# Kernel optimization log

Measured on AMD Instinct MI355X. Metric: run time of the kernel, lower is better.

The kernel has to match this reference:

```python
import jax, jax.numpy as jnp
import numpy as np

N_NODES = 100000
N_EDGES = 3200000
G_EDGES = 1600000
D_FEAT = 256
K_CLUSTERS = 16
COLLAPSE_REG = 0.1


def setup_inputs() -> dict:
    key = jax.random.key(0)
    ks = jax.random.split(key, 12)
    inp = {
        'features': jax.random.normal(ks[0], (N_NODES, D_FEAT), dtype=jnp.float32),
        'W': jax.random.normal(ks[1], (D_FEAT, K_CLUSTERS), dtype=jnp.float32) / np.sqrt(D_FEAT),
        'b': jnp.zeros((K_CLUSTERS,), dtype=jnp.float32),
        'adj_src': jax.random.randint(ks[2], (N_EDGES,), 0, N_NODES, dtype=jnp.int32),
        'adj_dst': jax.random.randint(ks[3], (N_EDGES,), 0, N_NODES, dtype=jnp.int32),
        'adj_val': jax.random.uniform(ks[4], (N_EDGES,), dtype=jnp.float32),
        'g1_src': jax.random.randint(ks[5], (G_EDGES,), 0, N_NODES, dtype=jnp.int32),
        'g1_dst': jax.random.randint(ks[6], (G_EDGES,), 0, N_NODES, dtype=jnp.int32),
        'g1_val': jax.random.uniform(ks[7], (G_EDGES,), dtype=jnp.float32),
        'g2_src': jax.random.randint(ks[8], (G_EDGES,), 0, N_NODES, dtype=jnp.int32),
        'g2_dst': jax.random.randint(ks[9], (G_EDGES,), 0, N_NODES, dtype=jnp.int32),
        'g2_val': jax.random.uniform(ks[10], (G_EDGES,), dtype=jnp.float32),
        'lamda': 1,
    }
    return inp


def _spmm(src, dst, val, X, n):
    # (sparse A) @ X where A[src, dst] = val : out[i] = sum_j A[i,j] X[j]
    return jax.ops.segment_sum(val[:, None] * X[dst], src, num_segments=n)


def _col_degrees(src, dst, val, n):
    # tf.sparse.reduce_sum(A, axis=0): column sums
    return jax.ops.segment_sum(val, dst, num_segments=n)


def reference(features, W, b, adj_src, adj_dst, adj_val,
              g1_src, g1_dst, g1_val, g2_src, g2_dst, g2_val, lamda):
    n = features.shape[0]
    k = W.shape[1]
    # soft cluster assignments  [n, k]
    S = jax.nn.softmax(features @ W + b, axis=1)
    cluster_sizes = jnp.sum(S, axis=0)            # [k]
    S_pool = S / cluster_sizes                    # [n, k]

    # full-graph modularity
    deg = _col_degrees(adj_src, adj_dst, adj_val, n)  # [n]
    m = jnp.sum(deg)                                  # total edge weight
    AS = _spmm(adj_src, adj_dst, adj_val, S, n)       # [n, k]
    graph_pooled = AS.T @ S                           # [k, k]
    dS = deg @ S                                      # [k] = S^T deg
    normalizer = jnp.outer(dS, dS) / 2.0 / m          # [k, k]
    spectral_loss = -jnp.trace(graph_pooled - normalizer) / 2.0 / m

    # per-group modularity Q_g
    def group_Q(src, dst, val):
        gdeg = _col_degrees(src, dst, val, n)
        gm = jnp.sum(gdeg)
        safe_gm = jnp.where(gm > 0, gm, 1.0)
        gAS = _spmm(src, dst, val, S, n)
        g_pooled = gAS.T @ S
        gdS = gdeg @ S
        g_norm = jnp.outer(gdS, gdS) / 2.0 / safe_gm
        Qg = jnp.trace(g_pooled - g_norm) / 2.0 / m
        return jnp.where(gm > 0, Qg, 0.0), gm

    Q1, m1 = group_Q(g1_src, g1_dst, g1_val)
    Q2, m2 = group_Q(g2_src, g2_dst, g2_val)
    Q_min = jnp.minimum(Q1, Q2)
    g_edges_mean = (m1 + m2) / 2.0
    edge_ratio = m / (g_edges_mean + 1e-8)
    fairness_loss = edge_ratio * (-Q_min)

    collapse_loss = (jnp.linalg.norm(cluster_sizes) / n) * jnp.sqrt(jnp.float32(k)) - 1.0

    total_loss = spectral_loss + lamda * fairness_loss + COLLAPSE_REG * collapse_loss

    features_pooled = jax.nn.selu(S_pool.T @ features)  # [k, d]
    return features_pooled, S, total_loss
```

## Files before the change

### kernel.cpp

```cpp
#include <hip/hip_runtime.h>
#include <cstddef>
#include <cstdint>


#define G1_MAX   1024
#define EGRID    2048
#define NSEG     16
#define OFF_E    0
#define SZ_E     (3 * 18 * EGRID)
#define OFF_R    (OFF_E + SZ_E)
#define OFF_G    (OFF_R + 4112)
#define OFF_F8   (OFF_G + 64)

#if __has_builtin(__builtin_amdgcn_cvt_pk_f32_fp8)
#define HW_FP8 1
#endif

__device__ __forceinline__ unsigned f32_to_e4m3(float f)
{
    unsigned bits = __float_as_uint(f);
    unsigned s = bits >> 31;
    int e32 = (int)((bits >> 23) & 255);
    unsigned m23 = bits & 0x7FFFFF;
    int e = e32 - 120;
    unsigned out;
    if (e32 == 0) out = 0;
    else if (e <= 0) {
        float av = fabsf(f);
        int q = (int)(av * 512.0f + 0.5f);
        out = (unsigned)q;
    } else if (e > 15) out = (15u << 3) | 6u;
    else {
        unsigned m3 = (m23 + 0x80000u) >> 20;
        if (m3 == 8u) { m3 = 0u; ++e; if (e > 15) { e = 15; m3 = 6u; } }
        out = ((unsigned)e << 3) | m3;
    }
    return out | (s << 7);
}

__device__ __forceinline__ void decode16(uint4 r, float* o, const float* lut)
{
#ifdef HW_FP8
    #pragma unroll
    for (int j = 0; j < 4; ++j) {
        unsigned u = (&r.x)[j];
        auto lo = __builtin_amdgcn_cvt_pk_f32_fp8(u, false);
        auto hi = __builtin_amdgcn_cvt_pk_f32_fp8(u, true);
        o[4*j]   = lo[0]; o[4*j+1] = lo[1];
        o[4*j+2] = hi[0]; o[4*j+3] = hi[1];
    }
#else
    #pragma unroll
    for (int j = 0; j < 4; ++j) {
        unsigned u = (&r.x)[j];
        #pragma unroll
        for (int q = 0; q < 4; ++q)
            o[4*j+q] = lut[(u >> (8*q)) & 255];
    }
#endif
}

__global__ void __launch_bounds__(256)
k_rows(const float* __restrict__ F, const float* __restrict__ W,
       const float* __restrict__ b, float* __restrict__ S_out,
       unsigned* __restrict__ S_f8, float* __restrict__ ws_P, int n, int n_tiles)
{
    __shared__ float Wt[16][260];
    __shared__ float rows[16][260];
    __shared__ float S_lds[16][17];
    __shared__ float cs_red[256];

    const int t = threadIdx.x;

    for (int idx = t; idx < 4096; idx += 256)
        Wt[idx & 15][idx >> 4] = W[idx];

    const float bk = b[t & 15];
    const int rl = t >> 4;
    const int kl = t & 15;
    const int kp = t & 15;
    const int cp = t >> 4;

    float4 P0 = {0,0,0,0}, P1 = {0,0,0,0}, P2 = {0,0,0,0}, P3 = {0,0,0,0};
    float cs_acc = 0.f;
    __syncthreads();

    for (int tile = blockIdx.x; tile < n_tiles; tile += gridDim.x) {
        const int row0 = tile << 4;
        const float4* F4 = (const float4*)(F + (size_t)row0 * 256);
        #pragma unroll
        for (int q = 0; q < 4; ++q) {
            int idx = t + (q << 8);
            int r = idx >> 6, dc = idx & 63;
            float4 v = {0.f, 0.f, 0.f, 0.f};
            if (row0 + r < n) v = F4[idx];
            *(float4*)&rows[r][dc << 2] = v;
        }
        __syncthreads();

        float acc = 0.f;
        #pragma unroll 8
        for (int dd = 0; dd < 64; ++dd) {
            float4 f4 = *(const float4*)&rows[rl][dd << 2];
            float4 w4 = *(const float4*)&Wt[kl][dd << 2];
            acc = fmaf(f4.x, w4.x, acc);
            acc = fmaf(f4.y, w4.y, acc);
            acc = fmaf(f4.z, w4.z, acc);
            acc = fmaf(f4.w, w4.w, acc);
        }
        acc += bk;

        float mx = acc;
        #pragma unroll
        for (int o = 8; o; o >>= 1) mx = fmaxf(mx, __shfl_xor(mx, o, 16));
        float ev = __expf(acc - mx);
        float sm = ev;
        #pragma unroll
        for (int o = 8; o; o >>= 1) sm += __shfl_xor(sm, o, 16);
        float sval = ev / sm;

        const bool valid = (row0 + rl) < n;
        if (valid) {
            S_out[(((size_t)(row0 + rl)) << 4) + kl] = sval;
            cs_acc += sval;
        }
        S_lds[rl][kl] = valid ? sval : 0.f;
        __syncthreads();

        if (t < 64) {
            int r = t >> 2, c = t & 3;
            int row = row0 + r;
            if (row < n) {
                unsigned u = f32_to_e4m3(S_lds[r][4*c])
                           | (f32_to_e4m3(S_lds[r][4*c+1]) << 8)
                           | (f32_to_e4m3(S_lds[r][4*c+2]) << 16)
                           | (f32_to_e4m3(S_lds[r][4*c+3]) << 24);
                S_f8[((size_t)row << 2) + c] = u;
            }
        }

        #pragma unroll 4
        for (int r = 0; r < 16; ++r) {
            float sv = S_lds[r][kp];
            const float* rp = &rows[r][cp << 4];
            float4 f0 = *(const float4*)&rp[0];
            float4 f1 = *(const float4*)&rp[4];
            float4 f2 = *(const float4*)&rp[8];
            float4 f3 = *(const float4*)&rp[12];
            P0.x = fmaf(sv, f0.x, P0.x); P0.y = fmaf(sv, f0.y, P0.y);
            P0.z = fmaf(sv, f0.z, P0.z); P0.w = fmaf(sv, f0.w, P0.w);
            P1.x = fmaf(sv, f1.x, P1.x); P1.y = fmaf(sv, f1.y, P1.y);
            P1.z = fmaf(sv, f1.z, P1.z); P1.w = fmaf(sv, f1.w, P1.w);
            P2.x = fmaf(sv, f2.x, P2.x); P2.y = fmaf(sv, f2.y, P2.y);
            P2.z = fmaf(sv, f2.z, P2.z); P2.w = fmaf(sv, f2.w, P2.w);
            P3.x = fmaf(sv, f3.x, P3.x); P3.y = fmaf(sv, f3.y, P3.y);
            P3.z = fmaf(sv, f3.z, P3.z); P3.w = fmaf(sv, f3.w, P3.w);
        }
        __syncthreads();
    }

    {
        float* dst = ws_P + (size_t)blockIdx.x * 4112 + kp * 256 + (cp << 4);
        *(float4*)&dst[0]  = P0;
        *(float4*)&dst[4]  = P1;
        *(float4*)&dst[8]  = P2;
        *(float4*)&dst[12] = P3;
    }
    cs_red[t] = cs_acc;
    __syncthreads();
    if (t < 16) {
        float ssum = 0.f;
        #pragma unroll
        for (int i = 0; i < 16; ++i) ssum += cs_red[t + (i << 4)];
        ws_P[(size_t)blockIdx.x * 4112 + 4096 + t] = ssum;
    }
}

__global__ void __launch_bounds__(256)
k_reduce(const float* __restrict__ ws_P, float* __restrict__ ws_red, int nb)
{
    const int seg  = blockIdx.x & (NSEG - 1);
    const int jblk = blockIdx.x / NSEG;
    const int idx  = jblk * 256 + threadIdx.x;
    if (idx >= 4112) return;
    const int chunk = (nb + NSEG - 1) / NSEG;
    const int b0 = seg * chunk;
    const int b1 = min(nb, b0 + chunk);
    float s = 0.f;
    for (int bb = b0; bb < b1; ++bb)
        s += ws_P[(size_t)bb * 4112 + idx];
    atomicAdd(&ws_red[idx], s);
}

__global__ void __launch_bounds__(256, 2)
k_edge(const int* __restrict__ src0, const int* __restrict__ dst0,
       const float* __restrict__ val0, int n0,
       const int* __restrict__ src1, const int* __restrict__ dst1,
       const float* __restrict__ val1, int n1,
       const int* __restrict__ src2, const int* __restrict__ dst2,
       const float* __restrict__ val2, int n2,
       const uint4* __restrict__ S8, float* __restrict__ ws_e,
       int b0, int b1)
{
#ifndef HW_FP8
    __shared__ float lut[256];
    if (threadIdx.x < 256) {
        int i = threadIdx.x;
        int e_ = (i >> 3) & 15, m_ = i & 7, s_ = i >> 7;
        float v = e_ ? ldexpf((float)(8 + m_), e_ - 10) : ldexpf((float)m_, -9);
        lut[i] = s_ ? -v : v;
    }
    __syncthreads();
    const float* lutp = lut;
#else
    const float* lutp = nullptr;
#endif

    int g, bb, nblk, nE;
    const int* src; const int* dst; const float* val;
    if ((int)blockIdx.x < b0)      { g = 0; bb = blockIdx.x;      nblk = b0;             src = src0; dst = dst0; val = val0; nE = n0; }
    else if ((int)blockIdx.x < b1) { g = 1; bb = blockIdx.x - b0; nblk = b1 - b0;        src = src1; dst = dst1; val = val1; nE = n1; }
    else                           { g = 2; bb = blockIdx.x - b1; nblk = gridDim.x - b1; src = src2; dst = dst2; val = val2; nE = n2; }

    float m_acc = 0.f, tr_acc = 0.f;
    float gds[16];
    #pragma unroll
    for (int k = 0; k < 16; ++k) gds[k] = 0.f;

    const int nv = nE >> 3;
    const int4*   s4 = (const int4*)src;
    const int4*   d4 = (const int4*)dst;
    const float4* v4 = (const float4*)val;
    const int stride = nblk * 256;

    for (int i = bb * 256 + threadIdx.x; i < nv; i += stride) {
        int4   sa = s4[2*i], sb = s4[2*i+1];
        int4   da = d4[2*i], db = d4[2*i+1];
        float4 va = v4[2*i], vb = v4[2*i+1];
        int   is[8] = {sa.x, sa.y, sa.z, sa.w, sb.x, sb.y, sb.z, sb.w};
        int   id[8] = {da.x, da.y, da.z, da.w, db.x, db.y, db.z, db.w};
        float vv[8] = {va.x, va.y, va.z, va.w, vb.x, vb.y, vb.z, vb.w};
        uint4 rs[8], rd[8];
        #pragma unroll
        for (int e = 0; e < 8; ++e) {
            rs[e] = S8[is[e]];
            rd[e] = S8[id[e]];
        }
        #pragma unroll
        for (int e = 0; e < 8; ++e) {
            float sv[16], dv[16];
            decode16(rs[e], sv, lutp);
            decode16(rd[e], dv, lutp);
            float v = vv[e];
            float dot = 0.f;
            #pragma unroll
            for (int k = 0; k < 16; ++k) dot = fmaf(sv[k], dv[k], dot);
            m_acc += v;
            tr_acc = fmaf(v, dot, tr_acc);
            #pragma unroll
            for (int k = 0; k < 16; ++k) gds[k] = fmaf(v, dv[k], gds[k]);
        }
    }

    if (bb == 0) {
        int e = (nv << 3) + threadIdx.x;
        if (e < nE) {
            float sv[16], dv[16];
            decode16(S8[src[e]], sv, lutp);
            decode16(S8[dst[e]], dv, lutp);
            float v = val[e];
            float dot = 0.f;
            #pragma unroll
            for (int k = 0; k < 16; ++k) dot = fmaf(sv[k], dv[k], dot);
            m_acc += v;
            tr_acc = fmaf(v, dot, tr_acc);
            #pragma unroll
            for (int k = 0; k < 16; ++k) gds[k] = fmaf(v, dv[k], gds[k]);
        }
    }

    #pragma unroll
    for (int o = 32; o; o >>= 1) {
        m_acc  += __shfl_xor(m_acc, o);
        tr_acc += __shfl_xor(tr_acc, o);
        #pragma unroll
        for (int k = 0; k < 16; ++k) gds[k] += __shfl_xor(gds[k], o);
    }
    __shared__ float wred[4][18];
    const int wid = threadIdx.x >> 6, lane = threadIdx.x & 63;
    if (lane == 0) {
        wred[wid][0] = m_acc; wred[wid][1] = tr_acc;
        #pragma unroll
        for (int k = 0; k < 16; ++k) wred[wid][2 + k] = gds[k];
    }
    __syncthreads();
    if (threadIdx.x < 18) {
        float s = wred[0][threadIdx.x] + wred[1][threadIdx.x]
                + wred[2][threadIdx.x] + wred[3][threadIdx.x];
        ws_e[(size_t)g * 18 * EGRID + (size_t)threadIdx.x * EGRID + bb] = s;
    }
}

__global__ void __launch_bounds__(256)
k_ereduce(const float* __restrict__ ws_e, float* __restrict__ G54,
          int g0, int g1, int g2)
{
    const int p = blockIdx.x;
    const int g = p / 18, slot = p % 18;
    int grids[3] = {g0, g1, g2};
    const int gb = grids[g];
    const float* base = ws_e + (size_t)g * 18 * EGRID + (size_t)slot * EGRID;

    const int t = threadIdx.x;
    float s = 0.f;
    for (int bb = t; bb < gb; bb += 256) s += base[bb];
    #pragma unroll
    for (int o = 32; o; o >>= 1) s += __shfl_xor(s, o);

    __shared__ float wr[4];
    if ((t & 63) == 0) wr[t >> 6] = s;
    __syncthreads();
    if (t == 0) G54[p] = wr[0] + wr[1] + wr[2] + wr[3];
}

__global__ void __launch_bounds__(256)
k_final(const float* __restrict__ ws_red, const float* __restrict__ G54,
        const void* __restrict__ lamda_ptr, float* __restrict__ out, int n)
{
    __shared__ float G[54];
    const int t = threadIdx.x;
    if (t < 54) G[t] = G54[t];
    __syncthreads();

    const float* P  = ws_red;
    const float* cs = ws_red + 4096;

    const float scale = 1.0507009873554805f;
    const float alpha = 1.6732632423543772f;
    for (int idx = t; idx < 4096; idx += 256) {
        int k = idx >> 8;
        float x = P[idx] / cs[k];
        float y = x > 0.f ? scale * x : scale * alpha * (expf(x) - 1.f);
        out[idx] = y;
    }

    if (t == 0) {
        int   li = *(const int*)lamda_ptr;
        float lf = *(const float*)lamda_ptr;
        float lamda = (li > -100000 && li < 100000) ? (float)li : lf;

        float m = G[0], trA = G[1];
        float ds2 = 0.f;
        for (int k = 0; k < 16; ++k) ds2 += G[2 + k] * G[2 + k];
        float spectral = -(trA - ds2 / (2.f * m)) / (2.f * m);

        float Q[2], gm[2];
        for (int g = 0; g < 2; ++g) {
            const float* Gg = G + 18 * (g + 1);
            float mg = Gg[0], trg = Gg[1];
            float gds2 = 0.f;
            for (int k = 0; k < 16; ++k) gds2 += Gg[2 + k] * Gg[2 + k];
            float safe = mg > 0.f ? mg : 1.f;
            float q = (trg - gds2 / (2.f * safe)) / (2.f * m);
            Q[g]  = mg > 0.f ? q : 0.f;
            gm[g] = mg;
        }
        float Qmin = fminf(Q[0], Q[1]);
        float gmean = 0.5f * (gm[0] + gm[1]);
        float fairness = (m / (gmean + 1e-8f)) * (-Qmin);

        float csn = 0.f;
        for (int k = 0; k < 16; ++k) csn += cs[k] * cs[k];
        float collapse = (sqrtf(csn) / (float)n) * 4.f - 1.f;

        out[4096 + (size_t)n * 16] = spectral + lamda * fairness + 0.1f * collapse;
    }
}

extern "C" void kernel_launch(void* const* d_in, const int* in_sizes, int n_in,
                              void* d_out, int out_size, void* d_ws, size_t ws_size,
                              hipStream_t stream)
{
    const float* F       = (const float*)d_in[0];
    const float* W       = (const float*)d_in[1];
    const float* b       = (const float*)d_in[2];
    const int*   adj_src = (const int*)d_in[3];
    const int*   adj_dst = (const int*)d_in[4];
    const float* adj_val = (const float*)d_in[5];
    const int*   g1_src  = (const int*)d_in[6];
    const int*   g1_dst  = (const int*)d_in[7];
    const float* g1_val  = (const float*)d_in[8];
    const int*   g2_src  = (const int*)d_in[9];
    const int*   g2_dst  = (const int*)d_in[10];
    const float* g2_val  = (const float*)d_in[11];
    const void*  lamda_p = d_in[12];

    const int n  = in_sizes[0] / 256;
    const int nE = in_sizes[3];
    const int n1 = in_sizes[6];
    const int n2 = in_sizes[9];

    float* out   = (float*)d_out;
    float* S_out = out + 4096;

    float* ws   = (float*)d_ws;
    float* ws_e = ws + OFF_E;
    float* ws_r = ws + OFF_R;
    float* ws_g = ws + OFF_G;
    unsigned* S8 = (unsigned*)(ws + OFF_F8);
    const size_t off_p = (size_t)OFF_F8 + (size_t)n * 4;
    float* ws_P = ws + off_p;

    const int n_tiles = (n + 15) >> 4;
    long avail = ((long)(ws_size / 4) - (long)off_p) / 4112;
    int grid1 = n_tiles < G1_MAX ? n_tiles : G1_MAX;
    if (avail < grid1) grid1 = (int)avail;
    if (grid1 < 1) grid1 = 1;

    hipMemsetAsync(ws_r, 0, 4112 * sizeof(float), stream);

    k_rows<<<grid1, 256, 0, stream>>>(F, W, b, S_out, S8, ws_P, n, n_tiles);
    k_reduce<<<17 * NSEG, 256, 0, stream>>>(ws_P, ws_r, grid1);

    auto eg = [](int ne) { int g = (ne / 8 + 255) / 256; if (g < 1) g = 1;
                           return g < EGRID ? g : EGRID; };
    const int b0 = eg(nE), b1g = eg(n1), b2g = eg(n2);
    k_edge<<<b0 + b1g + b2g, 256, 0, stream>>>(
        adj_src, adj_dst, adj_val, nE,
        g1_src, g1_dst, g1_val, n1,
        g2_src, g2_dst, g2_val, n2,
        (const uint4*)S8, ws_e, b0, b0 + b1g);

    k_ereduce<<<54, 256, 0, stream>>>(ws_e, ws_g, b0, b1g, b2g);
    k_final<<<1, 256, 0, stream>>>(ws_r, ws_g, lamda_p, out, n);
}
```

Before: 156.3 us.

## Stage feature tiles as bf16 in LDS with 32-row tiles; nontemporal edge loads

The row kernel now converts each feature tile to bf16 when writing it to LDS, stores W as bf16 too, and processes 32 rows per tile, with each thread computing two rows of logits. This cuts LDS footprint and LDS read traffic and halves the number of tile iterations and barriers. The edge kernel switches its streaming index and value loads to nontemporal loads to avoid polluting the cache that holds the gathered S rows. Rounding features and W to bf16 adds precision loss to the softmax logits and the pooled features.

Result: slower. 177.4 us (+13.5%).

```diff
diff --git a/kernel.cpp b/kernel.cpp
--- a/kernel.cpp
+++ b/kernel.cpp
@@ -12,9 +12,23 @@
 #define OFF_G    (OFF_R + 4112)
 #define OFF_F8   (OFF_G + 64)
 
+#define TROWS    32
+#define RPAD     280
+
+typedef int   iv4 __attribute__((ext_vector_type(4)));
+typedef float fv4 __attribute__((ext_vector_type(4)));
+
 #if __has_builtin(__builtin_amdgcn_cvt_pk_f32_fp8)
 #define HW_FP8 1
 #endif
+
+__device__ __forceinline__ unsigned bfr(float f)
+{
+    unsigned u = __float_as_uint(f);
+    return (u + 0x7FFFu + ((u >> 16) & 1u)) >> 16;
+}
+__device__ __forceinline__ float bf_lo(unsigned u) { return __uint_as_float(u << 16); }
+__device__ __forceinline__ float bf_hi(unsigned u) { return __uint_as_float(u & 0xFFFF0000u); }
 
 __device__ __forceinline__ unsigned f32_to_e4m3(float f)
 {
@@ -65,15 +79,15 @@
        const float* __restrict__ b, float* __restrict__ S_out,
        unsigned* __restrict__ S_f8, float* __restrict__ ws_P, int n, int n_tiles)
 {
-    __shared__ float Wt[16][260];
-    __shared__ float rows[16][260];
-    __shared__ float S_lds[16][17];
+    __shared__ unsigned short Wt_bf[16][RPAD];
+    __shared__ unsigned short rows_bf[TROWS][RPAD];
+    __shared__ float S_lds[TROWS][17];
     __shared__ float cs_red[256];
 
     const int t = threadIdx.x;
 
     for (int idx = t; idx < 4096; idx += 256)
-        Wt[idx & 15][idx >> 4] = W[idx];
+        Wt_bf[idx & 15][idx >> 4] = (unsigned short)bfr(W[idx]);
 
     const float bk = b[t & 15];
     const int rl = t >> 4;
@@ -86,48 +100,60 @@
     __syncthreads();
 
     for (int tile = blockIdx.x; tile < n_tiles; tile += gridDim.x) {
-        const int row0 = tile << 4;
+        const int row0 = tile * TROWS;
         const float4* F4 = (const float4*)(F + (size_t)row0 * 256);
         #pragma unroll
-        for (int q = 0; q < 4; ++q) {
+        for (int q = 0; q < 8; ++q) {
             int idx = t + (q << 8);
-            int r = idx >> 6, dc = idx & 63;
+            int r = idx >> 6, c4 = idx & 63;
             float4 v = {0.f, 0.f, 0.f, 0.f};
             if (row0 + r < n) v = F4[idx];
-            *(float4*)&rows[r][dc << 2] = v;
+            unsigned u0 = bfr(v.x) | (bfr(v.y) << 16);
+            unsigned u1 = bfr(v.z) | (bfr(v.w) << 16);
+            *(uint2*)&rows_bf[r][c4 << 2] = make_uint2(u0, u1);
         }
         __syncthreads();
 
-        float acc = 0.f;
+        float a0 = 0.f, a1 = 0.f;
         #pragma unroll 8
-        for (int dd = 0; dd < 64; ++dd) {
-            float4 f4 = *(const float4*)&rows[rl][dd << 2];
-            float4 w4 = *(const float4*)&Wt[kl][dd << 2];
-            acc = fmaf(f4.x, w4.x, acc);
-            acc = fmaf(f4.y, w4.y, acc);
-            acc = fmaf(f4.z, w4.z, acc);
-            acc = fmaf(f4.w, w4.w, acc);
-        }
-        acc += bk;
-
-        float mx = acc;
-        #pragma unroll
-        for (int o = 8; o; o >>= 1) mx = fmaxf(mx, __shfl_xor(mx, o, 16));
-        float ev = __expf(acc - mx);
-        float sm = ev;
-        #pragma unroll
-        for (int o = 8; o; o >>= 1) sm += __shfl_xor(sm, o, 16);
-        float sval = ev / sm;
-
-        const bool valid = (row0 + rl) < n;
-        if (valid) {
-            S_out[(((size_t)(row0 + rl)) << 4) + kl] = sval;
-            cs_acc += sval;
-        }
-        S_lds[rl][kl] = valid ? sval : 0.f;
+        for (int dd = 0; dd < 32; ++dd) {
+            uint4 wv = *(const uint4*)&Wt_bf[kl][dd << 3];
+            uint4 r0 = *(const uint4*)&rows_bf[rl][dd << 3];
+            uint4 r1 = *(const uint4*)&rows_bf[rl + 16][dd << 3];
+            #pragma unroll
+            for (int j = 0; j < 4; ++j) {
+                unsigned wu = (&wv.x)[j], u0 = (&r0.x)[j], u1 = (&r1.x)[j];
+                float wl = bf_lo(wu), wh = bf_hi(wu);
+                a0 = fmaf(bf_lo(u0), wl, a0); a0 = fmaf(bf_hi(u0), wh, a0);
+                a1 = fmaf(bf_lo(u1), wl, a1); a1 = fmaf(bf_hi(u1), wh, a1);
+            }
+        }
+        a0 += bk; a1 += bk;
+
+        float mx0 = a0, mx1 = a1;
+        #pragma unroll
+        for (int o = 8; o; o >>= 1) {
+            mx0 = fmaxf(mx0, __shfl_xor(mx0, o, 16));
+            mx1 = fmaxf(mx1, __shfl_xor(mx1, o, 16));
+        }
+        float e0 = __expf(a0 - mx0), e1 = __expf(a1 - mx1);
+        float s0 = e0, s1 = e1;
+        #pragma unroll
+        for (int o = 8; o; o >>= 1) {
+            s0 += __shfl_xor(s0, o, 16);
+            s1 += __shfl_xor(s1, o, 16);
+        }
+        float sv0 = e0 / s0, sv1 = e1 / s1;
+
+        const bool v0 = (row0 + rl) < n;
+        const bool v1 = (row0 + rl + 16) < n;
+        if (v0) { S_out[(((size_t)(row0 + rl)) << 4) + kl] = sv0; cs_acc += sv0; }
+        if (v1) { S_out[(((size_t)(row0 + rl + 16)) << 4) + kl] = sv1; cs_acc += sv1; }
+        S_lds[rl][kl]      = v0 ? sv0 : 0.f;
+        S_lds[rl + 16][kl] = v1 ? sv1 : 0.f;
         __syncthreads();
 
-        if (t < 64) {
+        if (t < 128) {
             int r = t >> 2, c = t & 3;
             int row = row0 + r;
             if (row < n) {
@@ -140,21 +166,27 @@
         }
 
         #pragma unroll 4
-        for (int r = 0; r < 16; ++r) {
+        for (int r = 0; r < TROWS; ++r) {
             float sv = S_lds[r][kp];
-            const float* rp = &rows[r][cp << 4];
-            float4 f0 = *(const float4*)&rp[0];
-            float4 f1 = *(const float4*)&rp[4];
-            float4 f2 = *(const float4*)&rp[8];
-            float4 f3 = *(const float4*)&rp[12];
-            P0.x = fmaf(sv, f0.x, P0.x); P0.y = fmaf(sv, f0.y, P0.y);
-            P0.z = fmaf(sv, f0.z, P0.z); P0.w = fmaf(sv, f0.w, P0.w);
-            P1.x = fmaf(sv, f1.x, P1.x); P1.y = fmaf(sv, f1.y, P1.y);
-            P1.z = fmaf(sv, f1.z, P1.z); P1.w = fmaf(sv, f1.w, P1.w);
-            P2.x = fmaf(sv, f2.x, P2.x); P2.y = fmaf(sv, f2.y, P2.y);
-            P2.z = fmaf(sv, f2.z, P2.z); P2.w = fmaf(sv, f2.w, P2.w);
-            P3.x = fmaf(sv, f3.x, P3.x); P3.y = fmaf(sv, f3.y, P3.y);
-            P3.z = fmaf(sv, f3.z, P3.z); P3.w = fmaf(sv, f3.w, P3.w);
+            const unsigned short* rp = &rows_bf[r][cp << 4];
+            uint4 fa = *(const uint4*)&rp[0];
+            uint4 fb = *(const uint4*)&rp[8];
+            float f0 = bf_lo(fa.x), f1 = bf_hi(fa.x);
+            float f2 = bf_lo(fa.y), f3 = bf_hi(fa.y);
+            float f4 = bf_lo(fa.z), f5 = bf_hi(fa.z);
+            float f6 = bf_lo(fa.w), f7 = bf_hi(fa.w);
+            float f8 = bf_lo(fb.x), f9 = bf_hi(fb.x);
+            float fA = bf_lo(fb.y), fB = bf_hi(fb.y);
+            float fC = bf_lo(fb.z), fD = bf_hi(fb.z);
+            float fE = bf_lo(fb.w), fF = bf_hi(fb.w);
+            P0.x = fmaf(sv, f0, P0.x); P0.y = fmaf(sv, f1, P0.y);
+            P0.z = fmaf(sv, f2, P0.z); P0.w = fmaf(sv, f3, P0.w);
+            P1.x = fmaf(sv, f4, P1.x); P1.y = fmaf(sv, f5, P1.y);
+            P1.z = fmaf(sv, f6, P1.z); P1.w = fmaf(sv, f7, P1.w);
+            P2.x = fmaf(sv, f8, P2.x); P2.y = fmaf(sv, f9, P2.y);
+            P2.z = fmaf(sv, fA, P2.z); P2.w = fmaf(sv, fB, P2.w);
+            P3.x = fmaf(sv, fC, P3.x); P3.y = fmaf(sv, fD, P3.y);
+            P3.z = fmaf(sv, fE, P3.z); P3.w = fmaf(sv, fF, P3.w);
         }
         __syncthreads();
     }
@@ -228,18 +260,21 @@
     for (int k = 0; k < 16; ++k) gds[k] = 0.f;
 
     const int nv = nE >> 3;
-    const int4*   s4 = (const int4*)src;
-    const int4*   d4 = (const int4*)dst;
-    const float4* v4 = (const float4*)val;
+    const iv4* s4 = (const iv4*)src;
+    const iv4* d4 = (const iv4*)dst;
+    const fv4* v4 = (const fv4*)val;
     const int stride = nblk * 256;
 
     for (int i = bb * 256 + threadIdx.x; i < nv; i += stride) {
-        int4   sa = s4[2*i], sb = s4[2*i+1];
-        int4   da = d4[2*i], db = d4[2*i+1];
-        float4 va = v4[2*i], vb = v4[2*i+1];
-        int   is[8] = {sa.x, sa.y, sa.z, sa.w, sb.x, sb.y, sb.z, sb.w};
-        int   id[8] = {da.x, da.y, da.z, da.w, db.x, db.y, db.z, db.w};
-        float vv[8] = {va.x, va.y, va.z, va.w, vb.x, vb.y, vb.z, vb.w};
+        iv4 sa = __builtin_nontemporal_load(&s4[2*i]);
+        iv4 sb = __builtin_nontemporal_load(&s4[2*i+1]);
+        iv4 da = __builtin_nontemporal_load(&d4[2*i]);
+        iv4 db = __builtin_nontemporal_load(&d4[2*i+1]);
+        fv4 va = __builtin_nontemporal_load(&v4[2*i]);
+        fv4 vb = __builtin_nontemporal_load(&v4[2*i+1]);
+        int   is[8] = {sa[0], sa[1], sa[2], sa[3], sb[0], sb[1], sb[2], sb[3]};
+        int   id[8] = {da[0], da[1], da[2], da[3], db[0], db[1], db[2], db[3]};
+        float vv[8] = {va[0], va[1], va[2], va[3], vb[0], vb[1], vb[2], vb[3]};
         uint4 rs[8], rd[8];
         #pragma unroll
         for (int e = 0; e < 8; ++e) {
@@ -411,13 +446,13 @@
     const size_t off_p = (size_t)OFF_F8 + (size_t)n * 4;
     float* ws_P = ws + off_p;
 
-    const int n_tiles = (n + 15) >> 4;
+    const int n_tiles = (n + TROWS - 1) / TROWS;
     long avail = ((long)(ws_size / 4) - (long)off_p) / 4112;
     int grid1 = n_tiles < G1_MAX ? n_tiles : G1_MAX;
     if (avail < grid1) grid1 = (int)avail;
     if (grid1 < 1) grid1 = 1;
 
-    hipMemsetAsync(ws_r, 0, 4112 * sizeof(float), stream);
+    (void)hipMemsetAsync(ws_r, 0, 4112 * sizeof(float), stream);
 
     k_rows<<<grid1, 256, 0, stream>>>(F, W, b, S_out, S8, ws_P, n, n_tiles);
     k_reduce<<<17 * NSEG, 256, 0, stream>>>(ws_P, ws_r, grid1);
```
